# Kernel optimization log

Hardware: AMD Instinct MI355X
Metric: run time of the kernel (lower is better)

The kernel has to match this reference:

```python
import jax, jax.numpy as jnp
import numpy as np

# Dims: batch=64, n_cols=512, n_e=80, n_i=20, embed=512
DT_OVER_TAU = 0.1  # leaky rate-neuron integration constant (dt/tau)

B, C, NE, NI, E = 64, 512, 80, 20, 512


def setup_inputs() -> dict:
    key = jax.random.key(0)
    ks = jax.random.split(key, 12)
    return {
        "thal": jax.random.normal(ks[0], (B, E), jnp.float32),
        "thal_increments": jax.random.normal(ks[1], (B, C, E), jnp.float32),
        "l23_fb": jax.random.normal(ks[2], (B, C, NE), jnp.float32),
        # state (rates nonnegative, membrane potentials gaussian)
        "r_e": jax.random.uniform(ks[3], (B, C, NE), jnp.float32),
        "r_i": jax.random.uniform(ks[4], (B, C, NI), jnp.float32),
        "e_v": jax.random.normal(ks[5], (B, C, NE), jnp.float32),
        "i_v": jax.random.normal(ks[6], (B, C, NI), jnp.float32),
        # learned params (per-column weight stacks)
        "input_proj": jax.random.normal(ks[7], (C, NE, E), jnp.float32) * (1.0 / np.sqrt(E).astype(np.float32)),
        "feedback_proj": jax.random.normal(ks[8], (C, NE, NE), jnp.float32) * (1.0 / np.sqrt(NE).astype(np.float32)),
        # static synapses: nonnegative weights, sign handled by E/I convention
        "W_ee": jax.random.uniform(ks[9], (C, NE, NE), jnp.float32) * (1.0 / np.sqrt(NE).astype(np.float32)),
        "W_ei": jax.random.uniform(ks[10], (C, NI, NE), jnp.float32) * (1.0 / np.sqrt(NE).astype(np.float32)),
        "W_ie": jax.random.uniform(ks[11], (C, NE, NI), jnp.float32) * (1.0 / np.sqrt(NI).astype(np.float32)),
    }


def reference(thal, thal_increments, l23_fb, r_e, r_i, e_v, i_v,
              input_proj, feedback_proj, W_ee, W_ei, W_ie):
    # thal [B,E] broadcast over columns + per-column increments -> [B,C,E]
    thal_full = thal[:, None, :] + thal_increments
    # external + feedback drive onto excitatory pop: [B,C,NE]
    I_ext = jnp.einsum('bce,coe->bco', thal_full, input_proj)
    I_fb = jnp.einsum('bce,coe->bco', l23_fb, feedback_proj)
    # synapse currents (static weights; E->E, E->I excitatory, I->E inhibitory)
    I_ee = jnp.einsum('bcp,cop->bco', r_e, W_ee)   # [B,C,NE]
    I_ei = jnp.einsum('bcp,cop->bco', r_e, W_ei)   # [B,C,NI]
    I_ie = -jnp.einsum('bcp,cop->bco', r_i, W_ie)  # [B,C,NE], inhibitory
    I_e_total = I_ext + I_fb + I_ee + I_ie
    I_i_total = I_ei
    # leaky rate-neuron state update: v <- v + dt/tau * (-v + I); r = relu(v)
    v_e_new = e_v + DT_OVER_TAU * (I_e_total - e_v)
    v_i_new = i_v + DT_OVER_TAU * (I_i_total - i_v)
    r_e_new = jax.nn.relu(v_e_new)
    r_i_new = jax.nn.relu(v_i_new)
    # (layer_outputs e_out/l23_out/l5_out all alias r_e_new; return new state too)
    return r_e_new, r_i_new, v_e_new, v_i_new
```

## Files before the change

### kernel.cpp

```cpp
#include <hip/hip_runtime.h>
#include <hip/hip_bf16.h>

typedef __attribute__((ext_vector_type(8))) short bf16x8;
typedef __attribute__((ext_vector_type(4))) float f32x4;
typedef unsigned short u16;
typedef unsigned int u32;

__device__ __forceinline__ u16 f2bf(float f) {
  __hip_bfloat16 h = __float2bfloat16(f);
  u16 u;
  __builtin_memcpy(&u, &h, 2);
  return u;
}
__device__ __forceinline__ void cvt4_store(u16* dst, float4 v) {
  u16 rr[4] = {f2bf(v.x), f2bf(v.y), f2bf(v.z), f2bf(v.w)};
  uint2 p;
  __builtin_memcpy(&p, rr, 8);
  *(uint2*)dst = p;
}


__global__ __launch_bounds__(256) void ei_cols_mfma(
    const float* __restrict__ thal,
    const float* __restrict__ inc,
    const float* __restrict__ l23,
    const float* __restrict__ re_in,
    const float* __restrict__ ri_in,
    const float* __restrict__ ev_in,
    const float* __restrict__ iv_in,
    const float* __restrict__ in_proj,
    const float* __restrict__ fb_proj,
    const float* __restrict__ w_ee,
    const float* __restrict__ w_ei,
    const float* __restrict__ w_ie,
    float* __restrict__ out)
{
  __shared__ __align__(16) unsigned char smem[41472];
  const int c = blockIdx.x;
  const int tid = threadIdx.x;
  const int lane = tid & 63;
  const int wave = tid >> 6;
  const int nidx = lane & 15;
  const int quad = lane >> 4;
  const int m0 = wave * 16;

  f32x4 acc_e[5], acc_i[2];
#pragma unroll
  for (int j = 0; j < 5; ++j) acc_e[j] = (f32x4){0.f, 0.f, 0.f, 0.f};
#pragma unroll
  for (int j = 0; j < 2; ++j) acc_i[j] = (f32x4){0.f, 0.f, 0.f, 0.f};

  {
    float4 tv[4], gv[4], wv[5];

    auto load_regs = [&](int k0) {
#pragma unroll
      for (int j = 0; j < 4; ++j) {
        int l = tid + j * 256;
        int b = l >> 4, kk = (l & 15) << 2;
        tv[j] = *(const float4*)(thal + b * 512 + k0 + kk);
        gv[j] = *(const float4*)(inc + (size_t)b * 262144 + (size_t)c * 512 + k0 + kk);
      }
#pragma unroll
      for (int j = 0; j < 5; ++j) {
        int l = tid + j * 256;
        int o = l >> 4, kk = (l & 15) << 2;
        wv[j] = *(const float4*)(in_proj + (size_t)c * 40960 + o * 512 + k0 + kk);
      }
    };
    auto store_buf = [&](int p) {
      u16* A = (u16*)(smem + p * 20736);
      u16* W = (u16*)(smem + 9216 + p * 20736);
#pragma unroll
      for (int j = 0; j < 4; ++j) {
        int l = tid + j * 256;
        int b = l >> 4, kk = (l & 15) << 2;
        float4 s;
        s.x = tv[j].x + gv[j].x; s.y = tv[j].y + gv[j].y;
        s.z = tv[j].z + gv[j].z; s.w = tv[j].w + gv[j].w;
        cvt4_store(A + b * 72 + kk, s);
      }
#pragma unroll
      for (int j = 0; j < 5; ++j) {
        int l = tid + j * 256;
        int o = l >> 4, kk = (l & 15) << 2;
        cvt4_store(W + o * 72 + kk, wv[j]);
      }
    };

    load_regs(0);
    store_buf(0);
    for (int i = 0; i < 8; ++i) {
      __syncthreads();
      if (i < 7) load_regs((i + 1) * 64);
      const int p = i & 1;
      u16* A = (u16*)(smem + p * 20736);
      u16* W = (u16*)(smem + 9216 + p * 20736);
#pragma unroll
      for (int kk0 = 0; kk0 < 64; kk0 += 32) {
        bf16x8 a = *(const bf16x8*)(A + (m0 + nidx) * 72 + kk0 + quad * 8);
#pragma unroll
        for (int j = 0; j < 5; ++j) {
          bf16x8 b = *(const bf16x8*)(W + (j * 16 + nidx) * 72 + kk0 + quad * 8);
          acc_e[j] = __builtin_amdgcn_mfma_f32_16x16x32_bf16(a, b, acc_e[j], 0, 0, 0);
        }
      }
      if (i < 7) store_buf((i + 1) & 1);
    }
  }

  {
    __syncthreads();
    u16* As = (u16*)smem;
    u16* Bs = (u16*)(smem + 13312);
    for (int l = tid; l < 1280; l += 256) {
      int b = l / 20, kk = (l % 20) << 2;
      cvt4_store(As + b * 104 + kk,
                 *(const float4*)(l23 + ((size_t)b * 512 + c) * 80 + kk));
    }
    for (int l = tid; l < 128; l += 256) {
      int b = l >> 1, off = 80 + (l & 1) * 8;
      *(uint4*)(As + b * 104 + off) = (uint4){0u, 0u, 0u, 0u};
    }
    for (int l = tid; l < 1600; l += 256) {
      int o = l / 20, kk = (l % 20) << 2;
      cvt4_store(Bs + o * 104 + kk,
                 *(const float4*)(fb_proj + ((size_t)c * 80 + o) * 80 + kk));
    }
    for (int l = tid; l < 160; l += 256) {
      int o = l >> 1, off = 80 + (l & 1) * 8;
      *(uint4*)(Bs + o * 104 + off) = (uint4){0u, 0u, 0u, 0u};
    }
    __syncthreads();
#pragma unroll
    for (int kk0 = 0; kk0 < 96; kk0 += 32) {
      bf16x8 a = *(const bf16x8*)(As + (m0 + nidx) * 104 + kk0 + quad * 8);
#pragma unroll
      for (int j = 0; j < 5; ++j) {
        bf16x8 b = *(const bf16x8*)(Bs + (j * 16 + nidx) * 104 + kk0 + quad * 8);
        acc_e[j] = __builtin_amdgcn_mfma_f32_16x16x32_bf16(a, b, acc_e[j], 0, 0, 0);
      }
    }
  }

  {
    __syncthreads();
    u16* As = (u16*)smem;
    u16* W1 = (u16*)(smem + 13312);
    u16* W2 = (u16*)(smem + 29952);
    for (int l = tid; l < 1280; l += 256) {
      int b = l / 20, kk = (l % 20) << 2;
      cvt4_store(As + b * 104 + kk,
                 *(const float4*)(re_in + ((size_t)b * 512 + c) * 80 + kk));
    }
    for (int l = tid; l < 128; l += 256) {
      int b = l >> 1, off = 80 + (l & 1) * 8;
      *(uint4*)(As + b * 104 + off) = (uint4){0u, 0u, 0u, 0u};
    }
    for (int l = tid; l < 1600; l += 256) {
      int o = l / 20, kk = (l % 20) << 2;
      cvt4_store(W1 + o * 104 + kk,
                 *(const float4*)(w_ee + ((size_t)c * 80 + o) * 80 + kk));
    }
    for (int l = tid; l < 160; l += 256) {
      int o = l >> 1, off = 80 + (l & 1) * 8;
      *(uint4*)(W1 + o * 104 + off) = (uint4){0u, 0u, 0u, 0u};
    }
    for (int l = tid; l < 400; l += 256) {
      int o = l / 20, kk = (l % 20) << 2;
      cvt4_store(W2 + o * 104 + kk,
                 *(const float4*)(w_ei + ((size_t)c * 20 + o) * 80 + kk));
    }
    for (int l = tid; l < 40; l += 256) {
      int o = l >> 1, off = 80 + (l & 1) * 8;
      *(uint4*)(W2 + o * 104 + off) = (uint4){0u, 0u, 0u, 0u};
    }
    for (int l = tid; l < 156; l += 256) {
      int o = 20 + l / 13, off = (l % 13) * 8;
      *(uint4*)(W2 + o * 104 + off) = (uint4){0u, 0u, 0u, 0u};
    }
    __syncthreads();
#pragma unroll
    for (int kk0 = 0; kk0 < 96; kk0 += 32) {
      bf16x8 a = *(const bf16x8*)(As + (m0 + nidx) * 104 + kk0 + quad * 8);
#pragma unroll
      for (int j = 0; j < 5; ++j) {
        bf16x8 b = *(const bf16x8*)(W1 + (j * 16 + nidx) * 104 + kk0 + quad * 8);
        acc_e[j] = __builtin_amdgcn_mfma_f32_16x16x32_bf16(a, b, acc_e[j], 0, 0, 0);
      }
#pragma unroll
      for (int j = 0; j < 2; ++j) {
        bf16x8 b = *(const bf16x8*)(W2 + (j * 16 + nidx) * 104 + kk0 + quad * 8);
        acc_i[j] = __builtin_amdgcn_mfma_f32_16x16x32_bf16(a, b, acc_i[j], 0, 0, 0);
      }
    }
  }

  {
    __syncthreads();
    u16* Ri = (u16*)smem;
    u16* Wn = (u16*)(smem + 5120);
    for (int l = tid; l < 320; l += 256) {
      int b = l / 5, kk = (l % 5) << 2;
      cvt4_store(Ri + b * 40 + kk,
                 *(const float4*)(ri_in + ((size_t)b * 512 + c) * 20 + kk));
    }
    for (int l = tid; l < 192; l += 256) {
      int b = l / 3, kk = 20 + (l % 3) * 4;
      *(uint2*)(Ri + b * 40 + kk) = (uint2){0u, 0u};
    }
    for (int l = tid; l < 400; l += 256) {
      int o = l / 5, kk = (l % 5) << 2;
      float4 v = *(const float4*)(w_ie + ((size_t)c * 80 + o) * 20 + kk);
      v.x = -v.x; v.y = -v.y; v.z = -v.z; v.w = -v.w;
      cvt4_store(Wn + o * 40 + kk, v);
    }
    for (int l = tid; l < 240; l += 256) {
      int o = l / 3, kk = 20 + (l % 3) * 4;
      *(uint2*)(Wn + o * 40 + kk) = (uint2){0u, 0u};
    }
    __syncthreads();
    {
      bf16x8 a = *(const bf16x8*)(Ri + (m0 + nidx) * 40 + quad * 8);
#pragma unroll
      for (int j = 0; j < 5; ++j) {
        bf16x8 b = *(const bf16x8*)(Wn + (j * 16 + nidx) * 40 + quad * 8);
        acc_e[j] = __builtin_amdgcn_mfma_f32_16x16x32_bf16(a, b, acc_e[j], 0, 0, 0);
      }
    }
  }

  __syncthreads();
  float* aE = (float*)smem;
  float* aI = (float*)(smem + 21504);
#pragma unroll
  for (int j = 0; j < 5; ++j)
#pragma unroll
    for (int r = 0; r < 4; ++r)
      aE[(m0 + quad * 4 + r) * 84 + j * 16 + nidx] = acc_e[j][r];
#pragma unroll
  for (int j = 0; j < 2; ++j) {
    int col = j * 16 + nidx;
    if (col < 20) {
#pragma unroll
      for (int r = 0; r < 4; ++r)
        aI[(m0 + quad * 4 + r) * 36 + col] = acc_i[j][r];
    }
  }
  __syncthreads();

  const size_t R_ri = 2621440u;
  const size_t R_ve = 3276800u;
  const size_t R_vi = 5898240u;
  for (int l = tid; l < 1280; l += 256) {
    int b = l / 20, c2 = (l % 20) << 2;
    float4 a = *(const float4*)(aE + b * 84 + c2);
    size_t g = ((size_t)b * 512 + c) * 80 + c2;
    float4 ev = *(const float4*)(ev_in + g);
    float4 v, r;
    v.x = ev.x + 0.1f * (a.x - ev.x); r.x = fmaxf(v.x, 0.f);
    v.y = ev.y + 0.1f * (a.y - ev.y); r.y = fmaxf(v.y, 0.f);
    v.z = ev.z + 0.1f * (a.z - ev.z); r.z = fmaxf(v.z, 0.f);
    v.w = ev.w + 0.1f * (a.w - ev.w); r.w = fmaxf(v.w, 0.f);
    *(float4*)(out + g) = r;
    *(float4*)(out + R_ve + g) = v;
  }
  for (int l = tid; l < 320; l += 256) {
    int b = l / 5, c2 = (l % 5) << 2;
    float4 a = *(const float4*)(aI + b * 36 + c2);
    size_t g = ((size_t)b * 512 + c) * 20 + c2;
    float4 iv = *(const float4*)(iv_in + g);
    float4 v, r;
    v.x = iv.x + 0.1f * (a.x - iv.x); r.x = fmaxf(v.x, 0.f);
    v.y = iv.y + 0.1f * (a.y - iv.y); r.y = fmaxf(v.y, 0.f);
    v.z = iv.z + 0.1f * (a.z - iv.z); r.z = fmaxf(v.z, 0.f);
    v.w = iv.w + 0.1f * (a.w - iv.w); r.w = fmaxf(v.w, 0.f);
    *(float4*)(out + R_ri + g) = r;
    *(float4*)(out + R_vi + g) = v;
  }
}

extern "C" void kernel_launch(void* const* d_in, const int* in_sizes, int n_in,
                              void* d_out, int out_size, void* d_ws, size_t ws_size,
                              hipStream_t stream) {
  const float* thal = (const float*)d_in[0];
  const float* inc = (const float*)d_in[1];
  const float* l23 = (const float*)d_in[2];
  const float* re = (const float*)d_in[3];
  const float* ri = (const float*)d_in[4];
  const float* ev = (const float*)d_in[5];
  const float* iv = (const float*)d_in[6];
  const float* in_proj = (const float*)d_in[7];
  const float* fb_proj = (const float*)d_in[8];
  const float* w_ee = (const float*)d_in[9];
  const float* w_ei = (const float*)d_in[10];
  const float* w_ie = (const float*)d_in[11];
  float* out = (float*)d_out;
  ei_cols_mfma<<<dim3(512), dim3(256), 0, stream>>>(
      thal, inc, l23, re, ri, ev, iv, in_proj, fb_proj, w_ee, w_ei, w_ie, out);
}
```

Before: 256.4 us.

## Split batch across two blocks per column and write outputs directly from registers

```diff
diff --git a/kernel.cpp b/kernel.cpp
--- a/kernel.cpp
+++ b/kernel.cpp
@@ -4,7 +4,6 @@
 typedef __attribute__((ext_vector_type(8))) short bf16x8;
 typedef __attribute__((ext_vector_type(4))) float f32x4;
 typedef unsigned short u16;
-typedef unsigned int u32;
 
 __device__ __forceinline__ u16 f2bf(float f) {
   __hip_bfloat16 h = __float2bfloat16(f);
@@ -20,7 +19,7 @@
 }
 
 
-__global__ __launch_bounds__(256) void ei_cols_mfma(
+__global__ __launch_bounds__(256, 4) void ei_cols_mfma(
     const float* __restrict__ thal,
     const float* __restrict__ inc,
     const float* __restrict__ l23,
@@ -35,31 +34,35 @@
     const float* __restrict__ w_ie,
     float* __restrict__ out)
 {
-  __shared__ __align__(16) unsigned char smem[41472];
+  __shared__ __align__(16) unsigned char smem[32256];
   const int c = blockIdx.x;
+  const int bh32 = blockIdx.y * 32;
   const int tid = threadIdx.x;
   const int lane = tid & 63;
   const int wave = tid >> 6;
   const int nidx = lane & 15;
   const int quad = lane >> 4;
-  const int m0 = wave * 16;
-
-  f32x4 acc_e[5], acc_i[2];
-#pragma unroll
-  for (int j = 0; j < 5; ++j) acc_e[j] = (f32x4){0.f, 0.f, 0.f, 0.f};
+  const int mw = wave & 1;
+  const int jh = wave >> 1;
+  const int m0 = mw * 16;
+
+  f32x4 acc_e[3], acc_i[2];
+#pragma unroll
+  for (int j = 0; j < 3; ++j) acc_e[j] = (f32x4){0.f, 0.f, 0.f, 0.f};
 #pragma unroll
   for (int j = 0; j < 2; ++j) acc_i[j] = (f32x4){0.f, 0.f, 0.f, 0.f};
 
   {
-    float4 tv[4], gv[4], wv[5];
+    float4 tv[2], gv[2], wv[5];
 
     auto load_regs = [&](int k0) {
 #pragma unroll
-      for (int j = 0; j < 4; ++j) {
+      for (int j = 0; j < 2; ++j) {
         int l = tid + j * 256;
         int b = l >> 4, kk = (l & 15) << 2;
-        tv[j] = *(const float4*)(thal + b * 512 + k0 + kk);
-        gv[j] = *(const float4*)(inc + (size_t)b * 262144 + (size_t)c * 512 + k0 + kk);
+        tv[j] = *(const float4*)(thal + (bh32 + b) * 512 + k0 + kk);
+        gv[j] = *(const float4*)(inc + (size_t)(bh32 + b) * 262144 +
+                                 (size_t)c * 512 + k0 + kk);
       }
 #pragma unroll
       for (int j = 0; j < 5; ++j) {
@@ -69,10 +72,10 @@
       }
     };
     auto store_buf = [&](int p) {
-      u16* A = (u16*)(smem + p * 20736);
-      u16* W = (u16*)(smem + 9216 + p * 20736);
-#pragma unroll
-      for (int j = 0; j < 4; ++j) {
+      u16* A = (u16*)(smem + p * 16128);
+      u16* W = (u16*)(smem + 4608 + p * 16128);
+#pragma unroll
+      for (int j = 0; j < 2; ++j) {
         int l = tid + j * 256;
         int b = l >> 4, kk = (l & 15) << 2;
         float4 s;
@@ -94,15 +97,23 @@
       __syncthreads();
       if (i < 7) load_regs((i + 1) * 64);
       const int p = i & 1;
-      u16* A = (u16*)(smem + p * 20736);
-      u16* W = (u16*)(smem + 9216 + p * 20736);
+      const u16* A = (const u16*)(smem + p * 16128);
+      const u16* W = (const u16*)(smem + 4608 + p * 16128);
 #pragma unroll
       for (int kk0 = 0; kk0 < 64; kk0 += 32) {
         bf16x8 a = *(const bf16x8*)(A + (m0 + nidx) * 72 + kk0 + quad * 8);
-#pragma unroll
-        for (int j = 0; j < 5; ++j) {
-          bf16x8 b = *(const bf16x8*)(W + (j * 16 + nidx) * 72 + kk0 + quad * 8);
-          acc_e[j] = __builtin_amdgcn_mfma_f32_16x16x32_bf16(a, b, acc_e[j], 0, 0, 0);
+        if (jh == 0) {
+#pragma unroll
+          for (int j = 0; j < 3; ++j) {
+            bf16x8 b = *(const bf16x8*)(W + (j * 16 + nidx) * 72 + kk0 + quad * 8);
+            acc_e[j] = __builtin_amdgcn_mfma_f32_16x16x32_bf16(a, b, acc_e[j], 0, 0, 0);
+          }
+        } else {
+#pragma unroll
+          for (int j = 0; j < 2; ++j) {
+            bf16x8 b = *(const bf16x8*)(W + ((j + 3) * 16 + nidx) * 72 + kk0 + quad * 8);
+            acc_e[j] = __builtin_amdgcn_mfma_f32_16x16x32_bf16(a, b, acc_e[j], 0, 0, 0);
+          }
         }
       }
       if (i < 7) store_buf((i + 1) & 1);
@@ -112,13 +123,13 @@
   {
     __syncthreads();
     u16* As = (u16*)smem;
-    u16* Bs = (u16*)(smem + 13312);
-    for (int l = tid; l < 1280; l += 256) {
+    u16* Bs = (u16*)(smem + 6656);
+    for (int l = tid; l < 640; l += 256) {
       int b = l / 20, kk = (l % 20) << 2;
       cvt4_store(As + b * 104 + kk,
-                 *(const float4*)(l23 + ((size_t)b * 512 + c) * 80 + kk));
-    }
-    for (int l = tid; l < 128; l += 256) {
+                 *(const float4*)(l23 + ((size_t)(bh32 + b) * 512 + c) * 80 + kk));
+    }
+    for (int l = tid; l < 64; l += 256) {
       int b = l >> 1, off = 80 + (l & 1) * 8;
       *(uint4*)(As + b * 104 + off) = (uint4){0u, 0u, 0u, 0u};
     }
@@ -135,10 +146,18 @@
 #pragma unroll
     for (int kk0 = 0; kk0 < 96; kk0 += 32) {
       bf16x8 a = *(const bf16x8*)(As + (m0 + nidx) * 104 + kk0 + quad * 8);
-#pragma unroll
-      for (int j = 0; j < 5; ++j) {
-        bf16x8 b = *(const bf16x8*)(Bs + (j * 16 + nidx) * 104 + kk0 + quad * 8);
-        acc_e[j] = __builtin_amdgcn_mfma_f32_16x16x32_bf16(a, b, acc_e[j], 0, 0, 0);
+      if (jh == 0) {
+#pragma unroll
+        for (int j = 0; j < 3; ++j) {
+          bf16x8 b = *(const bf16x8*)(Bs + (j * 16 + nidx) * 104 + kk0 + quad * 8);
+          acc_e[j] = __builtin_amdgcn_mfma_f32_16x16x32_bf16(a, b, acc_e[j], 0, 0, 0);
+        }
+      } else {
+#pragma unroll
+        for (int j = 0; j < 2; ++j) {
+          bf16x8 b = *(const bf16x8*)(Bs + ((j + 3) * 16 + nidx) * 104 + kk0 + quad * 8);
+          acc_e[j] = __builtin_amdgcn_mfma_f32_16x16x32_bf16(a, b, acc_e[j], 0, 0, 0);
+        }
       }
     }
   }
@@ -146,14 +165,14 @@
   {
     __syncthreads();
     u16* As = (u16*)smem;
-    u16* W1 = (u16*)(smem + 13312);
-    u16* W2 = (u16*)(smem + 29952);
-    for (int l = tid; l < 1280; l += 256) {
+    u16* W1 = (u16*)(smem + 6656);
+    u16* W2 = (u16*)(smem + 23296);
+    for (int l = tid; l < 640; l += 256) {
       int b = l / 20, kk = (l % 20) << 2;
       cvt4_store(As + b * 104 + kk,
-                 *(const float4*)(re_in + ((size_t)b * 512 + c) * 80 + kk));
-    }
-    for (int l = tid; l < 128; l += 256) {
+                 *(const float4*)(re_in + ((size_t)(bh32 + b) * 512 + c) * 80 + kk));
+    }
+    for (int l = tid; l < 64; l += 256) {
       int b = l >> 1, off = 80 + (l & 1) * 8;
       *(uint4*)(As + b * 104 + off) = (uint4){0u, 0u, 0u, 0u};
     }
@@ -175,37 +194,46 @@
       int o = l >> 1, off = 80 + (l & 1) * 8;
       *(uint4*)(W2 + o * 104 + off) = (uint4){0u, 0u, 0u, 0u};
     }
-    for (int l = tid; l < 156; l += 256) {
-      int o = 20 + l / 13, off = (l % 13) * 8;
+    for (int l = tid; l < 144; l += 256) {
+      int o = 20 + l / 12, off = (l % 12) * 8;
       *(uint4*)(W2 + o * 104 + off) = (uint4){0u, 0u, 0u, 0u};
     }
     __syncthreads();
 #pragma unroll
     for (int kk0 = 0; kk0 < 96; kk0 += 32) {
       bf16x8 a = *(const bf16x8*)(As + (m0 + nidx) * 104 + kk0 + quad * 8);
-#pragma unroll
-      for (int j = 0; j < 5; ++j) {
-        bf16x8 b = *(const bf16x8*)(W1 + (j * 16 + nidx) * 104 + kk0 + quad * 8);
-        acc_e[j] = __builtin_amdgcn_mfma_f32_16x16x32_bf16(a, b, acc_e[j], 0, 0, 0);
-      }
-#pragma unroll
-      for (int j = 0; j < 2; ++j) {
-        bf16x8 b = *(const bf16x8*)(W2 + (j * 16 + nidx) * 104 + kk0 + quad * 8);
-        acc_i[j] = __builtin_amdgcn_mfma_f32_16x16x32_bf16(a, b, acc_i[j], 0, 0, 0);
-      }
-    }
-  }
-
+      if (jh == 0) {
+#pragma unroll
+        for (int j = 0; j < 3; ++j) {
+          bf16x8 b = *(const bf16x8*)(W1 + (j * 16 + nidx) * 104 + kk0 + quad * 8);
+          acc_e[j] = __builtin_amdgcn_mfma_f32_16x16x32_bf16(a, b, acc_e[j], 0, 0, 0);
+        }
+      } else {
+#pragma unroll
+        for (int j = 0; j < 2; ++j) {
+          bf16x8 b = *(const bf16x8*)(W1 + ((j + 3) * 16 + nidx) * 104 + kk0 + quad * 8);
+          acc_e[j] = __builtin_amdgcn_mfma_f32_16x16x32_bf16(a, b, acc_e[j], 0, 0, 0);
+        }
+#pragma unroll
+        for (int j = 0; j < 2; ++j) {
+          bf16x8 b = *(const bf16x8*)(W2 + (j * 16 + nidx) * 104 + kk0 + quad * 8);
+          acc_i[j] = __builtin_amdgcn_mfma_f32_16x16x32_bf16(a, b, acc_i[j], 0, 0, 0);
+        }
+      }
+    }
+  }
+
+  float evr[3][4], ivr[2][4];
   {
     __syncthreads();
     u16* Ri = (u16*)smem;
-    u16* Wn = (u16*)(smem + 5120);
-    for (int l = tid; l < 320; l += 256) {
+    u16* Wn = (u16*)(smem + 2560);
+    for (int l = tid; l < 160; l += 256) {
       int b = l / 5, kk = (l % 5) << 2;
       cvt4_store(Ri + b * 40 + kk,
-                 *(const float4*)(ri_in + ((size_t)b * 512 + c) * 20 + kk));
-    }
-    for (int l = tid; l < 192; l += 256) {
+                 *(const float4*)(ri_in + ((size_t)(bh32 + b) * 512 + c) * 20 + kk));
+    }
+    for (int l = tid; l < 96; l += 256) {
       int b = l / 3, kk = 20 + (l % 3) * 4;
       *(uint2*)(Ri + b * 40 + kk) = (uint2){0u, 0u};
     }
@@ -219,64 +247,101 @@
       int o = l / 3, kk = 20 + (l % 3) * 4;
       *(uint2*)(Wn + o * 40 + kk) = (uint2){0u, 0u};
     }
+
+    {
+      const int row0 = bh32 + m0 + quad * 4;
+      if (jh == 0) {
+#pragma unroll
+        for (int j = 0; j < 3; ++j) {
+          int col = j * 16 + nidx;
+#pragma unroll
+          for (int r = 0; r < 4; ++r)
+            evr[j][r] = ev_in[((size_t)(row0 + r) * 512 + c) * 80 + col];
+        }
+      } else {
+#pragma unroll
+        for (int j = 0; j < 2; ++j) {
+          int col = (j + 3) * 16 + nidx;
+#pragma unroll
+          for (int r = 0; r < 4; ++r)
+            evr[j][r] = ev_in[((size_t)(row0 + r) * 512 + c) * 80 + col];
+        }
+#pragma unroll
+        for (int j = 0; j < 2; ++j) {
+          int col = j * 16 + nidx;
+#pragma unroll
+          for (int r = 0; r < 4; ++r)
+            ivr[j][r] = (col < 20)
+                ? iv_in[((size_t)(row0 + r) * 512 + c) * 20 + col] : 0.f;
+        }
+      }
+    }
+
     __syncthreads();
     {
       bf16x8 a = *(const bf16x8*)(Ri + (m0 + nidx) * 40 + quad * 8);
-#pragma unroll
-      for (int j = 0; j < 5; ++j) {
-        bf16x8 b = *(const bf16x8*)(Wn + (j * 16 + nidx) * 40 + quad * 8);
-        acc_e[j] = __builtin_amdgcn_mfma_f32_16x16x32_bf16(a, b, acc_e[j], 0, 0, 0);
-      }
-    }
-  }
-
-  __syncthreads();
-  float* aE = (float*)smem;
-  float* aI = (float*)(smem + 21504);
-#pragma unroll
-  for (int j = 0; j < 5; ++j)
-#pragma unroll
-    for (int r = 0; r < 4; ++r)
-      aE[(m0 + quad * 4 + r) * 84 + j * 16 + nidx] = acc_e[j][r];
-#pragma unroll
-  for (int j = 0; j < 2; ++j) {
-    int col = j * 16 + nidx;
-    if (col < 20) {
-#pragma unroll
-      for (int r = 0; r < 4; ++r)
-        aI[(m0 + quad * 4 + r) * 36 + col] = acc_i[j][r];
-    }
-  }
-  __syncthreads();
-
-  const size_t R_ri = 2621440u;
-  const size_t R_ve = 3276800u;
-  const size_t R_vi = 5898240u;
-  for (int l = tid; l < 1280; l += 256) {
-    int b = l / 20, c2 = (l % 20) << 2;
-    float4 a = *(const float4*)(aE + b * 84 + c2);
-    size_t g = ((size_t)b * 512 + c) * 80 + c2;
-    float4 ev = *(const float4*)(ev_in + g);
-    float4 v, r;
-    v.x = ev.x + 0.1f * (a.x - ev.x); r.x = fmaxf(v.x, 0.f);
-    v.y = ev.y + 0.1f * (a.y - ev.y); r.y = fmaxf(v.y, 0.f);
-    v.z = ev.z + 0.1f * (a.z - ev.z); r.z = fmaxf(v.z, 0.f);
-    v.w = ev.w + 0.1f * (a.w - ev.w); r.w = fmaxf(v.w, 0.f);
-    *(float4*)(out + g) = r;
-    *(float4*)(out + R_ve + g) = v;
-  }
-  for (int l = tid; l < 320; l += 256) {
-    int b = l / 5, c2 = (l % 5) << 2;
-    float4 a = *(const float4*)(aI + b * 36 + c2);
-    size_t g = ((size_t)b * 512 + c) * 20 + c2;
-    float4 iv = *(const float4*)(iv_in + g);
-    float4 v, r;
-    v.x = iv.x + 0.1f * (a.x - iv.x); r.x = fmaxf(v.x, 0.f);
-    v.y = iv.y + 0.1f * (a.y - iv.y); r.y = fmaxf(v.y, 0.f);
-    v.z = iv.z + 0.1f * (a.z - iv.z); r.z = fmaxf(v.z, 0.f);
-    v.w = iv.w + 0.1f * (a.w - iv.w); r.w = fmaxf(v.w, 0.f);
-    *(float4*)(out + R_ri + g) = r;
-    *(float4*)(out + R_vi + g) = v;
+      if (jh == 0) {
+#pragma unroll
+        for (int j = 0; j < 3; ++j) {
+          bf16x8 b = *(const bf16x8*)(Wn + (j * 16 + nidx) * 40 + quad * 8);
+          acc_e[j] = __builtin_amdgcn_mfma_f32_16x16x32_bf16(a, b, acc_e[j], 0, 0, 0);
+        }
+      } else {
+#pragma unroll
+        for (int j = 0; j < 2; ++j) {
+          bf16x8 b = *(const bf16x8*)(Wn + ((j + 3) * 16 + nidx) * 40 + quad * 8);
+          acc_e[j] = __builtin_amdgcn_mfma_f32_16x16x32_bf16(a, b, acc_e[j], 0, 0, 0);
+        }
+      }
+    }
+  }
+
+  {
+    const size_t R_ri = 2621440u;
+    const size_t R_ve = 3276800u;
+    const size_t R_vi = 5898240u;
+    const int row0 = bh32 + m0 + quad * 4;
+    if (jh == 0) {
+#pragma unroll
+      for (int j = 0; j < 3; ++j) {
+        int col = j * 16 + nidx;
+#pragma unroll
+        for (int r = 0; r < 4; ++r) {
+          size_t g = ((size_t)(row0 + r) * 512 + c) * 80 + col;
+          float e0 = evr[j][r];
+          float v = e0 + 0.1f * (acc_e[j][r] - e0);
+          out[g] = fmaxf(v, 0.f);
+          out[R_ve + g] = v;
+        }
+      }
+    } else {
+#pragma unroll
+      for (int j = 0; j < 2; ++j) {
+        int col = (j + 3) * 16 + nidx;
+#pragma unroll
+        for (int r = 0; r < 4; ++r) {
+          size_t g = ((size_t)(row0 + r) * 512 + c) * 80 + col;
+          float e0 = evr[j][r];
+          float v = e0 + 0.1f * (acc_e[j][r] - e0);
+          out[g] = fmaxf(v, 0.f);
+          out[R_ve + g] = v;
+        }
+      }
+#pragma unroll
+      for (int j = 0; j < 2; ++j) {
+        int col = j * 16 + nidx;
+        if (col < 20) {
+#pragma unroll
+          for (int r = 0; r < 4; ++r) {
+            size_t g = ((size_t)(row0 + r) * 512 + c) * 20 + col;
+            float i0 = ivr[j][r];
+            float v = i0 + 0.1f * (acc_i[j][r] - i0);
+            out[R_ri + g] = fmaxf(v, 0.f);
+            out[R_vi + g] = v;
+          }
+        }
+      }
+    }
   }
 }
 
@@ -296,6 +361,6 @@
   const float* w_ei = (const float*)d_in[10];
   const float* w_ie = (const float*)d_in[11];
   float* out = (float*)d_out;
-  ei_cols_mfma<<<dim3(512), dim3(256), 0, stream>>>(
+  ei_cols_mfma<<<dim3(512, 2), dim3(256), 0, stream>>>(
       thal, inc, l23, re, ri, ev, iv, in_proj, fb_proj, w_ee, w_ei, w_ie, out);
 }
```

After: 258.2 us. Within noise of the previous version (+0.7%).

## Stream all operands via direct global-to-LDS loads in a single double-buffered pipeline

Applied to the files above, without the earlier changes.

```diff
diff --git a/kernel.cpp b/kernel.cpp
--- a/kernel.cpp
+++ b/kernel.cpp
@@ -4,7 +4,6 @@
 typedef __attribute__((ext_vector_type(8))) short bf16x8;
 typedef __attribute__((ext_vector_type(4))) float f32x4;
 typedef unsigned short u16;
-typedef unsigned int u32;
 
 __device__ __forceinline__ u16 f2bf(float f) {
   __hip_bfloat16 h = __float2bfloat16(f);
@@ -12,15 +11,28 @@
   __builtin_memcpy(&u, &h, 2);
   return u;
 }
-__device__ __forceinline__ void cvt4_store(u16* dst, float4 v) {
-  u16 rr[4] = {f2bf(v.x), f2bf(v.y), f2bf(v.z), f2bf(v.w)};
-  uint2 p;
-  __builtin_memcpy(&p, rr, 8);
-  *(uint2*)dst = p;
-}
-
-
-__global__ __launch_bounds__(256) void ei_cols_mfma(
+__device__ __forceinline__ bf16x8 packv(f32x4 a, f32x4 b) {
+  u16 h[8] = {f2bf(a[0]), f2bf(a[1]), f2bf(a[2]), f2bf(a[3]),
+              f2bf(b[0]), f2bf(b[1]), f2bf(b[2]), f2bf(b[3])};
+  bf16x8 r;
+  __builtin_memcpy(&r, h, 16);
+  return r;
+}
+
+__device__ __forceinline__ void g2l(const float* g, char* l) {
+  __builtin_amdgcn_global_load_lds(
+      (const __attribute__((address_space(1))) void*)g,
+      (__attribute__((address_space(3))) void*)l, 16, 0, 0);
+}
+template <int N>
+__device__ __forceinline__ void waitvm() {
+  asm volatile("s_waitcnt vmcnt(%0)" ::"i"(N) : "memory");
+  __builtin_amdgcn_sched_barrier(0);
+}
+#define MFENCE() asm volatile("" ::: "memory")
+
+
+__global__ __launch_bounds__(256, 2) void ei_cols_mfma(
     const float* __restrict__ thal,
     const float* __restrict__ inc,
     const float* __restrict__ l23,
@@ -35,7 +47,8 @@
     const float* __restrict__ w_ie,
     float* __restrict__ out)
 {
-  __shared__ __align__(16) unsigned char smem[41472];
+  constexpr int BUF = 36864;
+  __shared__ __align__(16) char smem[2 * BUF];
   const int c = blockIdx.x;
   const int tid = threadIdx.x;
   const int lane = tid & 63;
@@ -43,6 +56,8 @@
   const int nidx = lane & 15;
   const int quad = lane >> 4;
   const int m0 = wave * 16;
+  const int brow = m0 + nidx;
+  const int q8 = quad * 8;
 
   f32x4 acc_e[5], acc_i[2];
 #pragma unroll
@@ -50,233 +65,343 @@
 #pragma unroll
   for (int j = 0; j < 2; ++j) acc_i[j] = (f32x4){0.f, 0.f, 0.f, 0.f};
 
+  auto bar = [&] { MFENCE(); __builtin_amdgcn_s_barrier(); MFENCE(); };
+
+  auto issueA = [&](int k0, int p) {
+    char* B = smem + p * BUF;
+#pragma unroll
+    for (int t = 0; t < 9; ++t) {
+      const int idx = wave * 9 + t;
+      const float* g;
+      if (idx < 16) {
+        const int L = idx * 64 + lane;
+        const int row = L >> 4, ch = (L & 15) ^ (row & 15);
+        g = inc + ((size_t)row * 512 + c) * 512 + k0 + (ch << 2);
+      } else {
+        const int L = (idx - 16) * 64 + lane;
+        const int row = L >> 4, ch = (L & 15) ^ (row & 15);
+        g = in_proj + (size_t)c * 40960 + (size_t)row * 512 + k0 + (ch << 2);
+      }
+      g2l(g, B + idx * 1024);
+    }
+  };
+  auto issue32 = [&](const float* aP, const float* bP, const float* iP,
+                     bool hasI, int kg, int p) {
+    char* B = smem + p * BUF;
+    const int n = hasI ? 6 : 5;
+    for (int t = 0; t < n; ++t) {
+      const int idx = wave * n + t;
+      const float* g;
+      if (idx < 8) {
+        const int L = idx * 64 + lane;
+        const int row = L >> 3, ch = (L & 7) ^ (row & 7);
+        g = aP + ((size_t)row * 512 + c) * 80 + kg + (ch << 2);
+      } else if (idx < 18) {
+        const int L = (idx - 8) * 64 + lane;
+        const int row = L >> 3, ch = (L & 7) ^ (row & 7);
+        g = bP + ((size_t)c * 80 + row) * 80 + kg + (ch << 2);
+      } else if (hasI && idx < 21) {
+        const int L = (idx - 18) * 64 + lane;
+        const int Lc = L < 160 ? L : 159;
+        const int row = Lc >> 3, ch = (Lc & 7) ^ (row & 7);
+        g = iP + ((size_t)c * 20 + row) * 80 + kg + (ch << 2);
+      } else {
+        g = thal + (lane << 2);
+      }
+      g2l(g, B + idx * 1024);
+    }
+  };
+  auto issue16 = [&](const float* aP, const float* bP, const float* iP,
+                     bool hasI, int p) {
+    char* B = smem + p * BUF;
+#pragma unroll
+    for (int t = 0; t < 3; ++t) {
+      const int idx = wave * 3 + t;
+      const float* g;
+      if (idx < 4) {
+        const int L = idx * 64 + lane;
+        const int row = L >> 2, ch = (L & 3) ^ (row & 3);
+        g = aP + ((size_t)row * 512 + c) * 80 + 64 + (ch << 2);
+      } else if (idx < 9) {
+        const int L = (idx - 4) * 64 + lane;
+        const int row = L >> 2, ch = (L & 3) ^ (row & 3);
+        g = bP + ((size_t)c * 80 + row) * 80 + 64 + (ch << 2);
+      } else if (hasI && idx < 11) {
+        const int L = (idx - 9) * 64 + lane;
+        const int Lc = L < 80 ? L : 79;
+        const int row = Lc >> 2, ch = (Lc & 3) ^ (row & 3);
+        g = iP + ((size_t)c * 20 + row) * 80 + 64 + (ch << 2);
+      } else {
+        g = thal + (lane << 2);
+      }
+      g2l(g, B + idx * 1024);
+    }
+  };
+  auto issueD = [&](int p) {
+    char* B = smem + p * BUF;
+#pragma unroll
+    for (int t = 0; t < 3; ++t) {
+      const int idx = wave * 3 + t;
+      const float* g;
+      if (idx < 5) {
+        const int L = idx * 64 + lane;
+        const int row = L / 5, ch = L % 5;
+        g = ri_in + ((size_t)row * 512 + c) * 20 + (ch << 2);
+      } else {
+        const int L = (idx - 5) * 64 + lane;
+        const int Lc = L < 400 ? L : 399;
+        const int row = Lc / 5, ch = Lc % 5;
+        g = w_ie + ((size_t)c * 80 + row) * 20 + (ch << 2);
+      }
+      g2l(g, B + idx * 1024);
+    }
+  };
+
+  auto computeA = [&](int p, const f32x4* tc) {
+    const float* As = (const float*)(smem + p * BUF);
+    const float* Ws = As + 4096;
+    const int rA = m0 + nidx;
+#pragma unroll
+    for (int h = 0; h < 2; ++h) {
+      const int c0 = h * 8 + quad * 2;
+      f32x4 a0 = *(const f32x4*)(As + rA * 64 + (((c0) ^ nidx) << 2));
+      f32x4 a1 = *(const f32x4*)(As + rA * 64 + (((c0 + 1) ^ nidx) << 2));
+      a0 += tc[2 * h];
+      a1 += tc[2 * h + 1];
+      bf16x8 af = packv(a0, a1);
+#pragma unroll
+      for (int j = 0; j < 5; ++j) {
+        const int rB = j * 16 + nidx;
+        f32x4 b0 = *(const f32x4*)(Ws + rB * 64 + (((c0) ^ nidx) << 2));
+        f32x4 b1 = *(const f32x4*)(Ws + rB * 64 + (((c0 + 1) ^ nidx) << 2));
+        acc_e[j] = __builtin_amdgcn_mfma_f32_16x16x32_bf16(af, packv(b0, b1),
+                                                           acc_e[j], 0, 0, 0);
+      }
+    }
+  };
+  auto compute32 = [&](int p, bool doI) {
+    const float* As = (const float*)(smem + p * BUF);
+    const float* Bs = As + 2048;
+    const float* Is = As + 4608;
+    const int s7 = nidx & 7;
+    const int c0 = quad * 2;
+    const int rA = m0 + nidx;
+    f32x4 a0 = *(const f32x4*)(As + rA * 32 + ((c0 ^ s7) << 2));
+    f32x4 a1 = *(const f32x4*)(As + rA * 32 + (((c0 + 1) ^ s7) << 2));
+    bf16x8 af = packv(a0, a1);
+#pragma unroll
+    for (int j = 0; j < 5; ++j) {
+      const int rB = j * 16 + nidx;
+      f32x4 b0 = *(const f32x4*)(Bs + rB * 32 + ((c0 ^ s7) << 2));
+      f32x4 b1 = *(const f32x4*)(Bs + rB * 32 + (((c0 + 1) ^ s7) << 2));
+      acc_e[j] = __builtin_amdgcn_mfma_f32_16x16x32_bf16(af, packv(b0, b1),
+                                                         acc_e[j], 0, 0, 0);
+    }
+    if (doI) {
+      f32x4 b0 = *(const f32x4*)(Is + nidx * 32 + ((c0 ^ s7) << 2));
+      f32x4 b1 = *(const f32x4*)(Is + nidx * 32 + (((c0 + 1) ^ s7) << 2));
+      acc_i[0] = __builtin_amdgcn_mfma_f32_16x16x32_bf16(af, packv(b0, b1),
+                                                         acc_i[0], 0, 0, 0);
+      f32x4 z = {0.f, 0.f, 0.f, 0.f};
+      f32x4 d0 = z, d1 = z;
+      if (nidx < 4) {
+        const int r6 = 16 + nidx;
+        d0 = *(const f32x4*)(Is + r6 * 32 + ((c0 ^ s7) << 2));
+        d1 = *(const f32x4*)(Is + r6 * 32 + (((c0 + 1) ^ s7) << 2));
+      }
+      acc_i[1] = __builtin_amdgcn_mfma_f32_16x16x32_bf16(af, packv(d0, d1),
+                                                         acc_i[1], 0, 0, 0);
+    }
+  };
+  auto compute16 = [&](int p, bool doI) {
+    const float* As = (const float*)(smem + p * BUF);
+    const float* Bs = As + 1024;
+    const float* Is = As + 2304;
+    const int s3 = nidx & 3;
+    const bool act = quad < 2;
+    const int c0 = quad * 2;
+    const int rA = m0 + nidx;
+    f32x4 z = {0.f, 0.f, 0.f, 0.f};
+    f32x4 a0 = z, a1 = z;
+    if (act) {
+      a0 = *(const f32x4*)(As + rA * 16 + ((c0 ^ s3) << 2));
+      a1 = *(const f32x4*)(As + rA * 16 + (((c0 + 1) ^ s3) << 2));
+    }
+    bf16x8 af = packv(a0, a1);
+#pragma unroll
+    for (int j = 0; j < 5; ++j) {
+      const int rB = j * 16 + nidx;
+      f32x4 b0 = z, b1 = z;
+      if (act) {
+        b0 = *(const f32x4*)(Bs + rB * 16 + ((c0 ^ s3) << 2));
+        b1 = *(const f32x4*)(Bs + rB * 16 + (((c0 + 1) ^ s3) << 2));
+      }
+      acc_e[j] = __builtin_amdgcn_mfma_f32_16x16x32_bf16(af, packv(b0, b1),
+                                                         acc_e[j], 0, 0, 0);
+    }
+    if (doI) {
+      f32x4 b0 = z, b1 = z;
+      if (act) {
+        b0 = *(const f32x4*)(Is + nidx * 16 + ((c0 ^ s3) << 2));
+        b1 = *(const f32x4*)(Is + nidx * 16 + (((c0 + 1) ^ s3) << 2));
+      }
+      acc_i[0] = __builtin_amdgcn_mfma_f32_16x16x32_bf16(af, packv(b0, b1),
+                                                         acc_i[0], 0, 0, 0);
+      f32x4 d0 = z, d1 = z;
+      if (act && nidx < 4) {
+        const int r6 = 16 + nidx;
+        d0 = *(const f32x4*)(Is + r6 * 16 + ((c0 ^ s3) << 2));
+        d1 = *(const f32x4*)(Is + r6 * 16 + (((c0 + 1) ^ s3) << 2));
+      }
+      acc_i[1] = __builtin_amdgcn_mfma_f32_16x16x32_bf16(af, packv(d0, d1),
+                                                         acc_i[1], 0, 0, 0);
+    }
+  };
+  auto computeD = [&](int p) {
+    const float* Ri = (const float*)(smem + p * BUF);
+    const float* Wn = Ri + 1280;
+    const int rA = m0 + nidx;
+    f32x4 z = {0.f, 0.f, 0.f, 0.f};
+    f32x4 a0 = z, a1 = z;
+    if (quad < 2) {
+      a0 = *(const f32x4*)(Ri + rA * 20 + q8);
+      a1 = *(const f32x4*)(Ri + rA * 20 + q8 + 4);
+    } else if (quad == 2) {
+      a0 = *(const f32x4*)(Ri + rA * 20 + 16);
+    }
+    bf16x8 af = packv(a0, a1);
+#pragma unroll
+    for (int j = 0; j < 5; ++j) {
+      const int rB = j * 16 + nidx;
+      f32x4 b0 = z, b1 = z;
+      if (quad < 2) {
+        b0 = *(const f32x4*)(Wn + rB * 20 + q8);
+        b1 = *(const f32x4*)(Wn + rB * 20 + q8 + 4);
+      } else if (quad == 2) {
+        b0 = *(const f32x4*)(Wn + rB * 20 + 16);
+      }
+      acc_e[j] = __builtin_amdgcn_mfma_f32_16x16x32_bf16(af, packv(-b0, -b1),
+                                                         acc_e[j], 0, 0, 0);
+    }
+  };
+
+  f32x4 tc[4], tn[4];
+  auto ldThal = [&](f32x4* t, int k0) {
+    const float* tb = thal + (size_t)brow * 512 + k0 + q8;
+    t[0] = *(const f32x4*)(tb);
+    t[1] = *(const f32x4*)(tb + 4);
+    t[2] = *(const f32x4*)(tb + 32);
+    t[3] = *(const f32x4*)(tb + 36);
+  };
+
+  float evr[5][4], ivr[2][4];
+  auto loadEV = [&] {
+    const int r0w = m0 + quad * 4;
+#pragma unroll
+    for (int j = 0; j < 5; ++j) {
+      const int col = j * 16 + nidx;
+#pragma unroll
+      for (int r = 0; r < 4; ++r)
+        evr[j][r] = ev_in[((size_t)(r0w + r) * 512 + c) * 80 + col];
+    }
+#pragma unroll
+    for (int r = 0; r < 4; ++r) {
+      ivr[0][r] = iv_in[((size_t)(r0w + r) * 512 + c) * 20 + nidx];
+      ivr[1][r] = 0.f;
+    }
+    if (nidx < 4) {
+#pragma unroll
+      for (int r = 0; r < 4; ++r)
+        ivr[1][r] = iv_in[((size_t)(r0w + r) * 512 + c) * 20 + 16 + nidx];
+    }
+  };
+
+  ldThal(tc, 0);
+  issueA(0, 0);
+#pragma unroll
+  for (int s = 0; s < 8; ++s) {
+    bar();
+    if (s < 7)
+      issueA((s + 1) * 64, (s + 1) & 1);
+    else
+      issue32(l23, fb_proj, nullptr, false, 0, 0);
+    if (s < 7)
+      waitvm<9>();
+    else
+      waitvm<5>();
+    bar();
+    if (s < 7) ldThal(tn, (s + 1) * 64);
+    computeA(s & 1, tc);
+#pragma unroll
+    for (int u = 0; u < 4; ++u) tc[u] = tn[u];
+  }
+  bar();
+  issue32(l23, fb_proj, nullptr, false, 32, 1);
+  waitvm<5>();
+  bar();
+  compute32(0, false);
+  bar();
+  issue16(l23, fb_proj, nullptr, false, 0);
+  waitvm<3>();
+  bar();
+  compute32(1, false);
+  bar();
+  issue32(re_in, w_ee, w_ei, true, 0, 1);
+  waitvm<6>();
+  bar();
+  compute16(0, false);
+  bar();
+  issue32(re_in, w_ee, w_ei, true, 32, 0);
+  waitvm<6>();
+  bar();
+  compute32(1, true);
+  bar();
+  issue16(re_in, w_ee, w_ei, true, 1);
+  waitvm<3>();
+  bar();
+  loadEV();
+  compute32(0, true);
+  bar();
+  issueD(0);
+  waitvm<3>();
+  bar();
+  compute16(1, true);
+  bar();
+  waitvm<0>();
+  bar();
+  computeD(0);
+
   {
-    float4 tv[4], gv[4], wv[5];
-
-    auto load_regs = [&](int k0) {
-#pragma unroll
-      for (int j = 0; j < 4; ++j) {
-        int l = tid + j * 256;
-        int b = l >> 4, kk = (l & 15) << 2;
-        tv[j] = *(const float4*)(thal + b * 512 + k0 + kk);
-        gv[j] = *(const float4*)(inc + (size_t)b * 262144 + (size_t)c * 512 + k0 + kk);
-      }
-#pragma unroll
-      for (int j = 0; j < 5; ++j) {
-        int l = tid + j * 256;
-        int o = l >> 4, kk = (l & 15) << 2;
-        wv[j] = *(const float4*)(in_proj + (size_t)c * 40960 + o * 512 + k0 + kk);
-      }
-    };
-    auto store_buf = [&](int p) {
-      u16* A = (u16*)(smem + p * 20736);
-      u16* W = (u16*)(smem + 9216 + p * 20736);
-#pragma unroll
-      for (int j = 0; j < 4; ++j) {
-        int l = tid + j * 256;
-        int b = l >> 4, kk = (l & 15) << 2;
-        float4 s;
-        s.x = tv[j].x + gv[j].x; s.y = tv[j].y + gv[j].y;
-        s.z = tv[j].z + gv[j].z; s.w = tv[j].w + gv[j].w;
-        cvt4_store(A + b * 72 + kk, s);
-      }
-#pragma unroll
-      for (int j = 0; j < 5; ++j) {
-        int l = tid + j * 256;
-        int o = l >> 4, kk = (l & 15) << 2;
-        cvt4_store(W + o * 72 + kk, wv[j]);
-      }
-    };
-
-    load_regs(0);
-    store_buf(0);
-    for (int i = 0; i < 8; ++i) {
-      __syncthreads();
-      if (i < 7) load_regs((i + 1) * 64);
-      const int p = i & 1;
-      u16* A = (u16*)(smem + p * 20736);
-      u16* W = (u16*)(smem + 9216 + p * 20736);
-#pragma unroll
-      for (int kk0 = 0; kk0 < 64; kk0 += 32) {
-        bf16x8 a = *(const bf16x8*)(A + (m0 + nidx) * 72 + kk0 + quad * 8);
-#pragma unroll
-        for (int j = 0; j < 5; ++j) {
-          bf16x8 b = *(const bf16x8*)(W + (j * 16 + nidx) * 72 + kk0 + quad * 8);
-          acc_e[j] = __builtin_amdgcn_mfma_f32_16x16x32_bf16(a, b, acc_e[j], 0, 0, 0);
+    const size_t R_ri = 2621440u;
+    const size_t R_ve = 3276800u;
+    const size_t R_vi = 5898240u;
+    const int r0w = m0 + quad * 4;
+#pragma unroll
+    for (int j = 0; j < 5; ++j) {
+      const int col = j * 16 + nidx;
+#pragma unroll
+      for (int r = 0; r < 4; ++r) {
+        size_t g = ((size_t)(r0w + r) * 512 + c) * 80 + col;
+        float e0 = evr[j][r];
+        float v = e0 + 0.1f * (acc_e[j][r] - e0);
+        out[g] = fmaxf(v, 0.f);
+        out[R_ve + g] = v;
+      }
+    }
+#pragma unroll
+    for (int jj = 0; jj < 2; ++jj) {
+      const int col = jj * 16 + nidx;
+      if (col < 20) {
+#pragma unroll
+        for (int r = 0; r < 4; ++r) {
+          size_t g = ((size_t)(r0w + r) * 512 + c) * 20 + col;
+          float i0 = ivr[jj][r];
+          float v = i0 + 0.1f * (acc_i[jj][r] - i0);
+          out[R_ri + g] = fmaxf(v, 0.f);
+          out[R_vi + g] = v;
         }
       }
-      if (i < 7) store_buf((i + 1) & 1);
-    }
-  }
-
-  {
-    __syncthreads();
-    u16* As = (u16*)smem;
-    u16* Bs = (u16*)(smem + 13312);
-    for (int l = tid; l < 1280; l += 256) {
-      int b = l / 20, kk = (l % 20) << 2;
-      cvt4_store(As + b * 104 + kk,
-                 *(const float4*)(l23 + ((size_t)b * 512 + c) * 80 + kk));
-    }
-    for (int l = tid; l < 128; l += 256) {
-      int b = l >> 1, off = 80 + (l & 1) * 8;
-      *(uint4*)(As + b * 104 + off) = (uint4){0u, 0u, 0u, 0u};
-    }
-    for (int l = tid; l < 1600; l += 256) {
-      int o = l / 20, kk = (l % 20) << 2;
-      cvt4_store(Bs + o * 104 + kk,
-                 *(const float4*)(fb_proj + ((size_t)c * 80 + o) * 80 + kk));
-    }
-    for (int l = tid; l < 160; l += 256) {
-      int o = l >> 1, off = 80 + (l & 1) * 8;
-      *(uint4*)(Bs + o * 104 + off) = (uint4){0u, 0u, 0u, 0u};
-    }
-    __syncthreads();
-#pragma unroll
-    for (int kk0 = 0; kk0 < 96; kk0 += 32) {
-      bf16x8 a = *(const bf16x8*)(As + (m0 + nidx) * 104 + kk0 + quad * 8);
-#pragma unroll
-      for (int j = 0; j < 5; ++j) {
-        bf16x8 b = *(const bf16x8*)(Bs + (j * 16 + nidx) * 104 + kk0 + quad * 8);
-        acc_e[j] = __builtin_amdgcn_mfma_f32_16x16x32_bf16(a, b, acc_e[j], 0, 0, 0);
-      }
-    }
-  }
-
-  {
-    __syncthreads();
-    u16* As = (u16*)smem;
-    u16* W1 = (u16*)(smem + 13312);
-    u16* W2 = (u16*)(smem + 29952);
-    for (int l = tid; l < 1280; l += 256) {
-      int b = l / 20, kk = (l % 20) << 2;
-      cvt4_store(As + b * 104 + kk,
-                 *(const float4*)(re_in + ((size_t)b * 512 + c) * 80 + kk));
-    }
-    for (int l = tid; l < 128; l += 256) {
-      int b = l >> 1, off = 80 + (l & 1) * 8;
-      *(uint4*)(As + b * 104 + off) = (uint4){0u, 0u, 0u, 0u};
-    }
-    for (int l = tid; l < 1600; l += 256) {
-      int o = l / 20, kk = (l % 20) << 2;
-      cvt4_store(W1 + o * 104 + kk,
-                 *(const float4*)(w_ee + ((size_t)c * 80 + o) * 80 + kk));
-    }
-    for (int l = tid; l < 160; l += 256) {
-      int o = l >> 1, off = 80 + (l & 1) * 8;
-      *(uint4*)(W1 + o * 104 + off) = (uint4){0u, 0u, 0u, 0u};
-    }
-    for (int l = tid; l < 400; l += 256) {
-      int o = l / 20, kk = (l % 20) << 2;
-      cvt4_store(W2 + o * 104 + kk,
-                 *(const float4*)(w_ei + ((size_t)c * 20 + o) * 80 + kk));
-    }
-    for (int l = tid; l < 40; l += 256) {
-      int o = l >> 1, off = 80 + (l & 1) * 8;
-      *(uint4*)(W2 + o * 104 + off) = (uint4){0u, 0u, 0u, 0u};
-    }
-    for (int l = tid; l < 156; l += 256) {
-      int o = 20 + l / 13, off = (l % 13) * 8;
-      *(uint4*)(W2 + o * 104 + off) = (uint4){0u, 0u, 0u, 0u};
-    }
-    __syncthreads();
-#pragma unroll
-    for (int kk0 = 0; kk0 < 96; kk0 += 32) {
-      bf16x8 a = *(const bf16x8*)(As + (m0 + nidx) * 104 + kk0 + quad * 8);
-#pragma unroll
-      for (int j = 0; j < 5; ++j) {
-        bf16x8 b = *(const bf16x8*)(W1 + (j * 16 + nidx) * 104 + kk0 + quad * 8);
-        acc_e[j] = __builtin_amdgcn_mfma_f32_16x16x32_bf16(a, b, acc_e[j], 0, 0, 0);
-      }
-#pragma unroll
-      for (int j = 0; j < 2; ++j) {
-        bf16x8 b = *(const bf16x8*)(W2 + (j * 16 + nidx) * 104 + kk0 + quad * 8);
-        acc_i[j] = __builtin_amdgcn_mfma_f32_16x16x32_bf16(a, b, acc_i[j], 0, 0, 0);
-      }
-    }
-  }
-
-  {
-    __syncthreads();
-    u16* Ri = (u16*)smem;
-    u16* Wn = (u16*)(smem + 5120);
-    for (int l = tid; l < 320; l += 256) {
-      int b = l / 5, kk = (l % 5) << 2;
-      cvt4_store(Ri + b * 40 + kk,
-                 *(const float4*)(ri_in + ((size_t)b * 512 + c) * 20 + kk));
-    }
-    for (int l = tid; l < 192; l += 256) {
-      int b = l / 3, kk = 20 + (l % 3) * 4;
-      *(uint2*)(Ri + b * 40 + kk) = (uint2){0u, 0u};
-    }
-    for (int l = tid; l < 400; l += 256) {
-      int o = l / 5, kk = (l % 5) << 2;
-      float4 v = *(const float4*)(w_ie + ((size_t)c * 80 + o) * 20 + kk);
-      v.x = -v.x; v.y = -v.y; v.z = -v.z; v.w = -v.w;
-      cvt4_store(Wn + o * 40 + kk, v);
-    }
-    for (int l = tid; l < 240; l += 256) {
-      int o = l / 3, kk = 20 + (l % 3) * 4;
-      *(uint2*)(Wn + o * 40 + kk) = (uint2){0u, 0u};
-    }
-    __syncthreads();
-    {
-      bf16x8 a = *(const bf16x8*)(Ri + (m0 + nidx) * 40 + quad * 8);
-#pragma unroll
-      for (int j = 0; j < 5; ++j) {
-        bf16x8 b = *(const bf16x8*)(Wn + (j * 16 + nidx) * 40 + quad * 8);
-        acc_e[j] = __builtin_amdgcn_mfma_f32_16x16x32_bf16(a, b, acc_e[j], 0, 0, 0);
-      }
-    }
-  }
-
-  __syncthreads();
-  float* aE = (float*)smem;
-  float* aI = (float*)(smem + 21504);
-#pragma unroll
-  for (int j = 0; j < 5; ++j)
-#pragma unroll
-    for (int r = 0; r < 4; ++r)
-      aE[(m0 + quad * 4 + r) * 84 + j * 16 + nidx] = acc_e[j][r];
-#pragma unroll
-  for (int j = 0; j < 2; ++j) {
-    int col = j * 16 + nidx;
-    if (col < 20) {
-#pragma unroll
-      for (int r = 0; r < 4; ++r)
-        aI[(m0 + quad * 4 + r) * 36 + col] = acc_i[j][r];
-    }
-  }
-  __syncthreads();
-
-  const size_t R_ri = 2621440u;
-  const size_t R_ve = 3276800u;
-  const size_t R_vi = 5898240u;
-  for (int l = tid; l < 1280; l += 256) {
-    int b = l / 20, c2 = (l % 20) << 2;
-    float4 a = *(const float4*)(aE + b * 84 + c2);
-    size_t g = ((size_t)b * 512 + c) * 80 + c2;
-    float4 ev = *(const float4*)(ev_in + g);
-    float4 v, r;
-    v.x = ev.x + 0.1f * (a.x - ev.x); r.x = fmaxf(v.x, 0.f);
-    v.y = ev.y + 0.1f * (a.y - ev.y); r.y = fmaxf(v.y, 0.f);
-    v.z = ev.z + 0.1f * (a.z - ev.z); r.z = fmaxf(v.z, 0.f);
-    v.w = ev.w + 0.1f * (a.w - ev.w); r.w = fmaxf(v.w, 0.f);
-    *(float4*)(out + g) = r;
-    *(float4*)(out + R_ve + g) = v;
-  }
-  for (int l = tid; l < 320; l += 256) {
-    int b = l / 5, c2 = (l % 5) << 2;
-    float4 a = *(const float4*)(aI + b * 36 + c2);
-    size_t g = ((size_t)b * 512 + c) * 20 + c2;
-    float4 iv = *(const float4*)(iv_in + g);
-    float4 v, r;
-    v.x = iv.x + 0.1f * (a.x - iv.x); r.x = fmaxf(v.x, 0.f);
-    v.y = iv.y + 0.1f * (a.y - iv.y); r.y = fmaxf(v.y, 0.f);
-    v.z = iv.z + 0.1f * (a.z - iv.z); r.z = fmaxf(v.z, 0.f);
-    v.w = iv.w + 0.1f * (a.w - iv.w); r.w = fmaxf(v.w, 0.f);
-    *(float4*)(out + R_ri + g) = r;
-    *(float4*)(out + R_vi + g) = v;
+    }
   }
 }
 
```

Result: no change. 256.8 us (+0.2%).
